# Optimization experiments

Hardware: AMD Instinct MI355X
Metric: run time of the kernel (lower is better)

The kernel has to match this reference:

```python
import jax, jax.numpy as jnp
import numpy as np

N_NODES = 50000
N_EDGES = 800000
D_FEAT = 128


def setup_inputs() -> dict:
    key = jax.random.key(0)
    k1, k2, k3, k4 = jax.random.split(key, 4)
    edge_index = jax.random.randint(k1, (2, N_EDGES), 0, N_NODES, dtype=jnp.int64 if jax.config.jax_enable_x64 else jnp.int32)
    edge_vals = jax.random.uniform(k2, (N_EDGES,), dtype=jnp.float32)
    features = jax.random.normal(k3, (N_NODES, D_FEAT), dtype=jnp.float32)
    bias = jax.random.normal(k4, (D_FEAT,), dtype=jnp.float32)
    return {"edge_index": edge_index, "edge_vals": edge_vals, "features": features, "bias": bias}


def reference(edge_index, edge_vals, features, bias):
    # SpMM: out[dst] += A[dst, src] * X[src], i.e. sparse adjacency @ dense features
    src = edge_index[0]
    dst = edge_index[1]
    msg = features[src] * edge_vals[:, None]          # [E, D] gather + scale
    out = jax.ops.segment_sum(msg, dst, num_segments=features.shape[0])  # [N, D] scatter-add
    return out + bias                                  # fused bias add
```

## Files before the change

### kernel.cpp

```cpp
#include <hip/hip_runtime.h>
#include <hip/hip_bf16.h>

#define D_FEAT 128
#define D4 (D_FEAT / 4)
#define BKT_SHIFT 7
#define BKT_NODES 128
#define NCHUNK 256
#define MAXBKT 512
#define CAP 3072

__global__ __launch_bounds__(256) void k1_hist_cvt(
        const int* __restrict__ dst, int E, int nbkt,
        int* __restrict__ M,
        const float4* __restrict__ fin, __hip_bfloat162* __restrict__ fout,
        int n4) {
    int c = blockIdx.x;
    int tid = threadIdx.x;
    if (c < NCHUNK) {
        __shared__ int hist[MAXBKT];
        for (int i = tid; i < MAXBKT; i += 256) hist[i] = 0;
        __syncthreads();
        int chunk = (E + NCHUNK - 1) / NCHUNK;
        int lo = c * chunk;
        int hi = min(lo + chunk, E);
        for (int i = lo + tid; i < hi; i += 256)
            atomicAdd(&hist[dst[i] >> BKT_SHIFT], 1);
        __syncthreads();
        for (int i = tid; i < MAXBKT; i += 256)
            M[c * MAXBKT + i] = hist[i];
    } else {
        int nb = gridDim.x - NCHUNK;
        int idx = (c - NCHUNK) * 256 + tid;
        int stride = nb * 256;
        for (int i = idx; i < n4; i += stride) {
            float4 f = fin[i];
            fout[2 * i + 0] = __float22bfloat162_rn(make_float2(f.x, f.y));
            fout[2 * i + 1] = __float22bfloat162_rn(make_float2(f.z, f.w));
        }
    }
}

__global__ __launch_bounds__(512) void k3_partition(
        const int* __restrict__ src, const int* __restrict__ dst,
        const float* __restrict__ vals, int E, int nbkt,
        const int* __restrict__ M, int* __restrict__ gbase,
        int2* __restrict__ spackA) {
    __shared__ int s[MAXBKT];
    __shared__ int lcur[MAXBKT];
    int c = blockIdx.x;
    int tid = threadIdx.x;
    int tot = 0, pre = 0;
    for (int cc = 0; cc < NCHUNK; ++cc) {
        int m = M[cc * MAXBKT + tid];
        tot += m;
        pre += (cc < c) ? m : 0;
    }
    s[tid] = tot;
    __syncthreads();
    for (int off = 1; off < MAXBKT; off <<= 1) {
        int t = (tid >= off) ? s[tid - off] : 0;
        __syncthreads();
        s[tid] += t;
        __syncthreads();
    }
    int incl = s[tid];
    int base = incl - tot;
    lcur[tid] = base + pre;
    if (c == 0) {
        if (tid < nbkt) gbase[tid] = base;
        if (tid == MAXBKT - 1) gbase[nbkt] = incl;
    }
    __syncthreads();
    int chunk = (E + NCHUNK - 1) / NCHUNK;
    int lo = c * chunk;
    int hi = min(lo + chunk, E);
    for (int i = lo + tid; i < hi; i += 512) {
        int d = dst[i];
        int pos = atomicAdd(&lcur[d >> BKT_SHIFT], 1);
        spackA[pos] = make_int2((src[i] & 0xFFFF) | ((d & (BKT_NODES - 1)) << 16),
                                __float_as_int(vals[i]));
    }
}

__global__ __launch_bounds__(1024) void k45_sort_gather(
        const int* __restrict__ gbase,
        const int2* __restrict__ spackA, int2* __restrict__ spackB,
        const __hip_bfloat162* __restrict__ feat,
        const float2* __restrict__ bias2, float2* __restrict__ out2,
        int N, int nbkt) {
    __shared__ int hist[BKT_NODES];
    __shared__ int sbuf[BKT_NODES];
    __shared__ int lcur[BKT_NODES];
    __shared__ int2 ls[CAP];
    int b = blockIdx.x;
    int tid = threadIdx.x;
    int base = gbase[b];
    int end  = gbase[b + 1];
    int cnt = end - base;
    bool inlds = (cnt <= CAP);

    if (tid < BKT_NODES) hist[tid] = 0;
    __syncthreads();
    for (int i = tid; i < cnt; i += 1024)
        atomicAdd(&hist[(spackA[base + i].x >> 16) & (BKT_NODES - 1)], 1);
    __syncthreads();
    if (tid < BKT_NODES) sbuf[tid] = hist[tid];
    __syncthreads();
    for (int off = 1; off < BKT_NODES; off <<= 1) {
        int t = (tid < BKT_NODES && tid >= off) ? sbuf[tid - off] : 0;
        __syncthreads();
        if (tid < BKT_NODES) sbuf[tid] += t;
        __syncthreads();
    }
    if (tid < BKT_NODES) lcur[tid] = sbuf[tid] - hist[tid];
    __syncthreads();
    for (int i = tid; i < cnt; i += 1024) {
        int2 r = spackA[base + i];
        int p = atomicAdd(&lcur[(r.x >> 16) & (BKT_NODES - 1)], 1);
        if (inlds) ls[p] = r;
        else       spackB[base + p] = r;
    }
    __syncthreads();

    int wave = tid >> 6, lane = tid & 63;
    float2 bv = bias2[lane];
    for (int n = wave; n < BKT_NODES; n += 16) {
        int node = (b << BKT_SHIFT) + n;
        if (node >= N) break;
        int lbeg = sbuf[n] - hist[n];
        int lend = sbuf[n];
        float2 acc0 = bv;
        float2 acc1 = make_float2(0.f, 0.f);
        int e = lbeg;
        if (inlds) {
            for (; e + 8 <= lend; e += 8) {
                int2 p[8];
                __hip_bfloat162 h[8];
#pragma unroll
                for (int j = 0; j < 8; j++) p[j] = ls[e + j];
#pragma unroll
                for (int j = 0; j < 8; j++)
                    h[j] = feat[(size_t)(p[j].x & 0xFFFF) * 64 + lane];
#pragma unroll
                for (int j = 0; j < 8; j++) {
                    float v = __int_as_float(p[j].y);
                    float2 f = __bfloat1622float2(h[j]);
                    if (j & 1) { acc1.x += v * f.x; acc1.y += v * f.y; }
                    else       { acc0.x += v * f.x; acc0.y += v * f.y; }
                }
            }
            for (; e < lend; e++) {
                int2 p = ls[e];
                float v = __int_as_float(p.y);
                float2 f = __bfloat1622float2(feat[(size_t)(p.x & 0xFFFF) * 64 + lane]);
                acc0.x += v * f.x; acc0.y += v * f.y;
            }
        } else {
            for (; e + 8 <= lend; e += 8) {
                int2 p[8];
                __hip_bfloat162 h[8];
#pragma unroll
                for (int j = 0; j < 8; j++) p[j] = spackB[base + e + j];
#pragma unroll
                for (int j = 0; j < 8; j++)
                    h[j] = feat[(size_t)(p[j].x & 0xFFFF) * 64 + lane];
#pragma unroll
                for (int j = 0; j < 8; j++) {
                    float v = __int_as_float(p[j].y);
                    float2 f = __bfloat1622float2(h[j]);
                    if (j & 1) { acc1.x += v * f.x; acc1.y += v * f.y; }
                    else       { acc0.x += v * f.x; acc0.y += v * f.y; }
                }
            }
            for (; e < lend; e++) {
                int2 p = spackB[base + e];
                float v = __int_as_float(p.y);
                float2 f = __bfloat1622float2(feat[(size_t)(p.x & 0xFFFF) * 64 + lane]);
                acc0.x += v * f.x; acc0.y += v * f.y;
            }
        }
        acc0.x += acc1.x; acc0.y += acc1.y;
        out2[(size_t)node * 64 + lane] = acc0;
    }
}


__global__ void init_bias_kernel(float4* __restrict__ out,
                                 const float4* __restrict__ bias, int n4) {
    int i = blockIdx.x * blockDim.x + threadIdx.x;
    if (i < n4) out[i] = bias[i & (D4 - 1)];
}

__global__ void spmm_edge_kernel(const int* __restrict__ src,
                                 const int* __restrict__ dst,
                                 const float* __restrict__ vals,
                                 const float4* __restrict__ feat,
                                 float* __restrict__ out, int n_edges) {
    int tid = blockIdx.x * blockDim.x + threadIdx.x;
    int e = tid >> 5;
    int lane = tid & 31;
    if (e >= n_edges) return;
    int s = src[e];
    int d = dst[e];
    float v = vals[e];
    float4 f = feat[(size_t)s * D4 + lane];
    float* o = out + (size_t)d * D_FEAT + lane * 4;
    atomicAdd(o + 0, v * f.x);
    atomicAdd(o + 1, v * f.y);
    atomicAdd(o + 2, v * f.z);
    atomicAdd(o + 3, v * f.w);
}

extern "C" void kernel_launch(void* const* d_in, const int* in_sizes, int n_in,
                              void* d_out, int out_size, void* d_ws, size_t ws_size,
                              hipStream_t stream) {
    const int* edge_index = (const int*)d_in[0];
    const float* edge_vals = (const float*)d_in[1];
    const float* features  = (const float*)d_in[2];
    const float* bias      = (const float*)d_in[3];

    int E = in_sizes[1];
    int N = in_sizes[2] / D_FEAT;
    const int* src = edge_index;
    const int* dst = edge_index + E;
    float* out = (float*)d_out;

    int nbkt = (N + BKT_NODES - 1) >> BKT_SHIFT;
    int n4 = N * D_FEAT / 4;

    size_t fb_bytes = (size_t)N * D_FEAT * 2;
    size_t sp_bytes = (size_t)E * 8;
    size_t m_bytes  = (size_t)NCHUNK * MAXBKT * 4;
    size_t needed = fb_bytes + 2 * sp_bytes + m_bytes + (MAXBKT + 1) * 4;

    bool ok = (ws_size >= needed) && (N >= 1) && (N <= 65536) && (E >= 1) &&
              (in_sizes[3] == D_FEAT) && (nbkt <= MAXBKT);

    if (ok) {
        char* wp = (char*)d_ws;
        __hip_bfloat162* fb16 = (__hip_bfloat162*)wp;  wp += fb_bytes;
        int2* spackA = (int2*)wp;                      wp += sp_bytes;
        int2* spackB = (int2*)wp;                      wp += sp_bytes;
        int* M       = (int*)wp;                       wp += m_bytes;
        int* gbase   = (int*)wp;

        k1_hist_cvt<<<NCHUNK + 256, 256, 0, stream>>>(dst, E, nbkt, M,
                                                      (const float4*)features,
                                                      fb16, n4);
        k3_partition<<<NCHUNK, 512, 0, stream>>>(src, dst, edge_vals, E,
                                                 nbkt, M, gbase, spackA);
        k45_sort_gather<<<nbkt, 1024, 0, stream>>>(gbase, spackA, spackB,
                                                   fb16, (const float2*)bias,
                                                   (float2*)out, N, nbkt);
    } else {
        int no4 = out_size / 4;
        {
            int block = 256, grid = (no4 + block - 1) / block;
            init_bias_kernel<<<grid, block, 0, stream>>>((float4*)out,
                                                         (const float4*)bias, no4);
        }
        {
            int block = 256;
            long long total = (long long)E * 32;
            int grid = (int)((total + block - 1) / block);
            spmm_edge_kernel<<<grid, block, 0, stream>>>(src, dst, edge_vals,
                                                         (const float4*)features,
                                                         out, E);
        }
    }
}
```

Before: 152.5 us.

## Replace bucketed two-level sort with per-node counting sort via global atomics

Swaps the bucket histogram, partition and in-LDS per-bucket sort for a direct per-node CSR build. A global atomic histogram over destination nodes is followed by a block scan and an atomic-cursor scatter, and a grid-stride gather then handles one node per wave. This drops the second sort pass and the spackB buffer, but relies on heavily contended global atomics (800k atomics on 50k counters, twice) and scatters writes randomly. The gather loop now pads partial groups of eight with masked loads.

```diff
diff --git a/kernel.cpp b/kernel.cpp
--- a/kernel.cpp
+++ b/kernel.cpp
@@ -3,35 +3,22 @@
 
 #define D_FEAT 128
 #define D4 (D_FEAT / 4)
-#define BKT_SHIFT 7
-#define BKT_NODES 128
-#define NCHUNK 256
-#define MAXBKT 512
-#define CAP 3072
+#define MAXBLK 64
 
 __global__ __launch_bounds__(256) void k1_hist_cvt(
-        const int* __restrict__ dst, int E, int nbkt,
-        int* __restrict__ M,
+        const int* __restrict__ dst, int E,
+        int* __restrict__ cnt,
         const float4* __restrict__ fin, __hip_bfloat162* __restrict__ fout,
         int n4) {
     int c = blockIdx.x;
     int tid = threadIdx.x;
-    if (c < NCHUNK) {
-        __shared__ int hist[MAXBKT];
-        for (int i = tid; i < MAXBKT; i += 256) hist[i] = 0;
-        __syncthreads();
-        int chunk = (E + NCHUNK - 1) / NCHUNK;
-        int lo = c * chunk;
-        int hi = min(lo + chunk, E);
-        for (int i = lo + tid; i < hi; i += 256)
-            atomicAdd(&hist[dst[i] >> BKT_SHIFT], 1);
-        __syncthreads();
-        for (int i = tid; i < MAXBKT; i += 256)
-            M[c * MAXBKT + i] = hist[i];
+    if (c < 256) {
+        int idx = c * 256 + tid;
+        for (int i = idx; i < E; i += 256 * 256)
+            atomicAdd(&cnt[dst[i]], 1);
     } else {
-        int nb = gridDim.x - NCHUNK;
-        int idx = (c - NCHUNK) * 256 + tid;
-        int stride = nb * 256;
+        int idx = (c - 256) * 256 + tid;
+        int stride = (gridDim.x - 256) * 256;
         for (int i = idx; i < n4; i += stride) {
             float4 f = fin[i];
             fout[2 * i + 0] = __float22bfloat162_rn(make_float2(f.x, f.y));
@@ -40,147 +27,97 @@
     }
 }
 
-__global__ __launch_bounds__(512) void k3_partition(
-        const int* __restrict__ src, const int* __restrict__ dst,
-        const float* __restrict__ vals, int E, int nbkt,
-        const int* __restrict__ M, int* __restrict__ gbase,
-        int2* __restrict__ spackA) {
-    __shared__ int s[MAXBKT];
-    __shared__ int lcur[MAXBKT];
-    int c = blockIdx.x;
-    int tid = threadIdx.x;
-    int tot = 0, pre = 0;
-    for (int cc = 0; cc < NCHUNK; ++cc) {
-        int m = M[cc * MAXBKT + tid];
-        tot += m;
-        pre += (cc < c) ? m : 0;
-    }
-    s[tid] = tot;
+__global__ __launch_bounds__(1024) void k2_scan(const int* __restrict__ cnt,
+                                                int* __restrict__ cursor,
+                                                int* __restrict__ bsum) {
+    __shared__ int s[1024];
+    int tid = threadIdx.x;
+    int j = blockIdx.x * 1024 + tid;
+    int v = cnt[j];
+    s[tid] = v;
     __syncthreads();
-    for (int off = 1; off < MAXBKT; off <<= 1) {
+    for (int off = 1; off < 1024; off <<= 1) {
         int t = (tid >= off) ? s[tid - off] : 0;
         __syncthreads();
         s[tid] += t;
         __syncthreads();
     }
-    int incl = s[tid];
-    int base = incl - tot;
-    lcur[tid] = base + pre;
-    if (c == 0) {
-        if (tid < nbkt) gbase[tid] = base;
-        if (tid == MAXBKT - 1) gbase[nbkt] = incl;
-    }
+    cursor[j] = s[tid] - v;
+    if (tid == 1023) bsum[blockIdx.x] = s[1023];
+}
+
+__device__ inline void scan_bsum(const int* __restrict__ bsum, int nblk,
+                                 int* sb, int tid) {
+    if (tid < 64) {
+        int v0 = (tid < nblk) ? bsum[tid] : 0;
+        int v = v0;
+        for (int off = 1; off < 64; off <<= 1) {
+            int t = __shfl_up(v, off, 64);
+            if (tid >= off) v += t;
+        }
+        sb[tid] = v - v0;
+    }
+}
+
+__global__ __launch_bounds__(1024) void k3_scatter(
+        const int* __restrict__ src, const int* __restrict__ dst,
+        const float* __restrict__ vals, int E, int nblk,
+        const int* __restrict__ bsum, int* __restrict__ cursor,
+        int2* __restrict__ spack) {
+    __shared__ int sb[MAXBLK];
+    int tid = threadIdx.x;
+    scan_bsum(bsum, nblk, sb, tid);
     __syncthreads();
-    int chunk = (E + NCHUNK - 1) / NCHUNK;
-    int lo = c * chunk;
-    int hi = min(lo + chunk, E);
-    for (int i = lo + tid; i < hi; i += 512) {
+    int idx = blockIdx.x * 1024 + tid;
+    int stride = gridDim.x * 1024;
+    for (int i = idx; i < E; i += stride) {
         int d = dst[i];
-        int pos = atomicAdd(&lcur[d >> BKT_SHIFT], 1);
-        spackA[pos] = make_int2((src[i] & 0xFFFF) | ((d & (BKT_NODES - 1)) << 16),
-                                __float_as_int(vals[i]));
-    }
-}
-
-__global__ __launch_bounds__(1024) void k45_sort_gather(
-        const int* __restrict__ gbase,
-        const int2* __restrict__ spackA, int2* __restrict__ spackB,
-        const __hip_bfloat162* __restrict__ feat,
-        const float2* __restrict__ bias2, float2* __restrict__ out2,
-        int N, int nbkt) {
-    __shared__ int hist[BKT_NODES];
-    __shared__ int sbuf[BKT_NODES];
-    __shared__ int lcur[BKT_NODES];
-    __shared__ int2 ls[CAP];
-    int b = blockIdx.x;
-    int tid = threadIdx.x;
-    int base = gbase[b];
-    int end  = gbase[b + 1];
-    int cnt = end - base;
-    bool inlds = (cnt <= CAP);
-
-    if (tid < BKT_NODES) hist[tid] = 0;
+        int pos = sb[d >> 10] + atomicAdd(&cursor[d], 1);
+        spack[pos] = make_int2(src[i], __float_as_int(vals[i]));
+    }
+}
+
+__global__ __launch_bounds__(1024) void k45_gather(
+        const int* __restrict__ cnt, const int* __restrict__ cursor,
+        const int* __restrict__ bsum, int nblk,
+        const int2* __restrict__ spack, const __hip_bfloat162* __restrict__ feat,
+        const float2* __restrict__ bias2, float2* __restrict__ out2, int N) {
+    __shared__ int sb[MAXBLK];
+    int tid = threadIdx.x;
+    scan_bsum(bsum, nblk, sb, tid);
     __syncthreads();
-    for (int i = tid; i < cnt; i += 1024)
-        atomicAdd(&hist[(spackA[base + i].x >> 16) & (BKT_NODES - 1)], 1);
-    __syncthreads();
-    if (tid < BKT_NODES) sbuf[tid] = hist[tid];
-    __syncthreads();
-    for (int off = 1; off < BKT_NODES; off <<= 1) {
-        int t = (tid < BKT_NODES && tid >= off) ? sbuf[tid - off] : 0;
-        __syncthreads();
-        if (tid < BKT_NODES) sbuf[tid] += t;
-        __syncthreads();
-    }
-    if (tid < BKT_NODES) lcur[tid] = sbuf[tid] - hist[tid];
-    __syncthreads();
-    for (int i = tid; i < cnt; i += 1024) {
-        int2 r = spackA[base + i];
-        int p = atomicAdd(&lcur[(r.x >> 16) & (BKT_NODES - 1)], 1);
-        if (inlds) ls[p] = r;
-        else       spackB[base + p] = r;
-    }
-    __syncthreads();
-
-    int wave = tid >> 6, lane = tid & 63;
+    int lane = tid & 63;
+    int w = blockIdx.x * (blockDim.x >> 6) + (tid >> 6);
+    int nw = gridDim.x * (blockDim.x >> 6);
     float2 bv = bias2[lane];
-    for (int n = wave; n < BKT_NODES; n += 16) {
-        int node = (b << BKT_SHIFT) + n;
-        if (node >= N) break;
-        int lbeg = sbuf[n] - hist[n];
-        int lend = sbuf[n];
+    for (int n = w; n < N; n += nw) {
+        int c = cnt[n];
+        int endl = cursor[n];
+        int start = sb[n >> 10] + endl - c;
+        int fin = start + c;
         float2 acc0 = bv;
         float2 acc1 = make_float2(0.f, 0.f);
-        int e = lbeg;
-        if (inlds) {
-            for (; e + 8 <= lend; e += 8) {
-                int2 p[8];
-                __hip_bfloat162 h[8];
+        for (int g = 0; g < c; g += 8) {
+            int2 p[8];
+            __hip_bfloat162 h[8];
 #pragma unroll
-                for (int j = 0; j < 8; j++) p[j] = ls[e + j];
+            for (int j = 0; j < 8; j++) {
+                int ei = start + g + j;
+                p[j] = spack[min(ei, fin - 1)];
+            }
 #pragma unroll
-                for (int j = 0; j < 8; j++)
-                    h[j] = feat[(size_t)(p[j].x & 0xFFFF) * 64 + lane];
+            for (int j = 0; j < 8; j++)
+                h[j] = feat[(size_t)(unsigned)p[j].x * 64 + lane];
 #pragma unroll
-                for (int j = 0; j < 8; j++) {
-                    float v = __int_as_float(p[j].y);
-                    float2 f = __bfloat1622float2(h[j]);
-                    if (j & 1) { acc1.x += v * f.x; acc1.y += v * f.y; }
-                    else       { acc0.x += v * f.x; acc0.y += v * f.y; }
-                }
+            for (int j = 0; j < 8; j++) {
+                float v = (start + g + j < fin) ? __int_as_float(p[j].y) : 0.f;
+                float2 f = __bfloat1622float2(h[j]);
+                if (j & 1) { acc1.x += v * f.x; acc1.y += v * f.y; }
+                else       { acc0.x += v * f.x; acc0.y += v * f.y; }
             }
-            for (; e < lend; e++) {
-                int2 p = ls[e];
-                float v = __int_as_float(p.y);
-                float2 f = __bfloat1622float2(feat[(size_t)(p.x & 0xFFFF) * 64 + lane]);
-                acc0.x += v * f.x; acc0.y += v * f.y;
-            }
-        } else {
-            for (; e + 8 <= lend; e += 8) {
-                int2 p[8];
-                __hip_bfloat162 h[8];
-#pragma unroll
-                for (int j = 0; j < 8; j++) p[j] = spackB[base + e + j];
-#pragma unroll
-                for (int j = 0; j < 8; j++)
-                    h[j] = feat[(size_t)(p[j].x & 0xFFFF) * 64 + lane];
-#pragma unroll
-                for (int j = 0; j < 8; j++) {
-                    float v = __int_as_float(p[j].y);
-                    float2 f = __bfloat1622float2(h[j]);
-                    if (j & 1) { acc1.x += v * f.x; acc1.y += v * f.y; }
-                    else       { acc0.x += v * f.x; acc0.y += v * f.y; }
-                }
-            }
-            for (; e < lend; e++) {
-                int2 p = spackB[base + e];
-                float v = __int_as_float(p.y);
-                float2 f = __bfloat1622float2(feat[(size_t)(p.x & 0xFFFF) * 64 + lane]);
-                acc0.x += v * f.x; acc0.y += v * f.y;
-            }
         }
         acc0.x += acc1.x; acc0.y += acc1.y;
-        out2[(size_t)node * 64 + lane] = acc0;
+        out2[(size_t)n * 64 + lane] = acc0;
     }
 }
 
@@ -225,33 +162,34 @@
     const int* dst = edge_index + E;
     float* out = (float*)d_out;
 
-    int nbkt = (N + BKT_NODES - 1) >> BKT_SHIFT;
+    int NPAD = ((N + 1023) / 1024) * 1024;
+    int nblk = NPAD / 1024;
     int n4 = N * D_FEAT / 4;
 
     size_t fb_bytes = (size_t)N * D_FEAT * 2;
     size_t sp_bytes = (size_t)E * 8;
-    size_t m_bytes  = (size_t)NCHUNK * MAXBKT * 4;
-    size_t needed = fb_bytes + 2 * sp_bytes + m_bytes + (MAXBKT + 1) * 4;
+    size_t needed = fb_bytes + sp_bytes + (size_t)NPAD * 8 + MAXBLK * 4;
 
     bool ok = (ws_size >= needed) && (N >= 1) && (N <= 65536) && (E >= 1) &&
-              (in_sizes[3] == D_FEAT) && (nbkt <= MAXBKT);
+              (in_sizes[3] == D_FEAT) && (nblk <= MAXBLK);
 
     if (ok) {
         char* wp = (char*)d_ws;
         __hip_bfloat162* fb16 = (__hip_bfloat162*)wp;  wp += fb_bytes;
-        int2* spackA = (int2*)wp;                      wp += sp_bytes;
-        int2* spackB = (int2*)wp;                      wp += sp_bytes;
-        int* M       = (int*)wp;                       wp += m_bytes;
-        int* gbase   = (int*)wp;
-
-        k1_hist_cvt<<<NCHUNK + 256, 256, 0, stream>>>(dst, E, nbkt, M,
-                                                      (const float4*)features,
-                                                      fb16, n4);
-        k3_partition<<<NCHUNK, 512, 0, stream>>>(src, dst, edge_vals, E,
-                                                 nbkt, M, gbase, spackA);
-        k45_sort_gather<<<nbkt, 1024, 0, stream>>>(gbase, spackA, spackB,
-                                                   fb16, (const float2*)bias,
-                                                   (float2*)out, N, nbkt);
+        int2* spack = (int2*)wp;                       wp += sp_bytes;
+        int* cnt    = (int*)wp;                        wp += (size_t)NPAD * 4;
+        int* cursor = (int*)wp;                        wp += (size_t)NPAD * 4;
+        int* bsum   = (int*)wp;
+
+        hipMemsetAsync(cnt, 0, (size_t)NPAD * 4, stream);
+        k1_hist_cvt<<<512, 256, 0, stream>>>(dst, E, cnt,
+                                             (const float4*)features, fb16, n4);
+        k2_scan<<<nblk, 1024, 0, stream>>>(cnt, cursor, bsum);
+        k3_scatter<<<256, 1024, 0, stream>>>(src, dst, edge_vals, E, nblk,
+                                             bsum, cursor, spack);
+        k45_gather<<<256, 1024, 0, stream>>>(cnt, cursor, bsum, nblk,
+                                             spack, fb16, (const float2*)bias,
+                                             (float2*)out, N);
     } else {
         int no4 = out_size / 4;
         {
```

New measurement: 225.9 us. 1.48x slower.
